# Kernel optimization log

Hardware: AMD Instinct MI355X
Metric: run time of the kernel (lower is better)

Reference implementation:

```python
import jax, jax.numpy as jnp
import numpy as np

N_NODES = 50000
N_EDGES = 600000
HIDDEN = 128
HEADS = 8
OUT_CH = HIDDEN // HEADS
NUM_LAYERS = 3
NEG_SLOPE = 0.2   # PyG GATConv default leaky_relu slope
BN_EPS = 1e-5

# Note: dropout is a no-op in eval mode; BatchNorm uses batch statistics
# (training-mode math, the only well-defined choice without running stats).

def setup_inputs() -> dict:
    key = jax.random.key(0)
    ks = jax.random.split(key, 9)
    x = jax.random.normal(ks[0], (N_NODES, HIDDEN), dtype=jnp.float32)
    edge_index = jax.random.randint(ks[1], (2, N_EDGES), 0, N_NODES, dtype=jnp.int64)
    s = 1.0 / np.sqrt(HIDDEN)
    W = jax.random.normal(ks[2], (NUM_LAYERS, HIDDEN, HEADS * OUT_CH), dtype=jnp.float32) * s
    att_src = jax.random.normal(ks[3], (NUM_LAYERS, HEADS, OUT_CH), dtype=jnp.float32) * s
    att_dst = jax.random.normal(ks[4], (NUM_LAYERS, HEADS, OUT_CH), dtype=jnp.float32) * s
    bias = jnp.zeros((NUM_LAYERS, HIDDEN), dtype=jnp.float32)
    gamma = jnp.ones((NUM_LAYERS, HIDDEN), dtype=jnp.float32)
    beta = jnp.zeros((NUM_LAYERS, HIDDEN), dtype=jnp.float32)
    return {"x": x, "edge_index": edge_index, "W": W, "att_src": att_src,
            "att_dst": att_dst, "bias": bias, "gamma": gamma, "beta": beta}


def _gat_layer(x, src, dst, W, a_src, a_dst, b):
    n = x.shape[0]
    h = (x @ W).reshape(n, HEADS, OUT_CH)              # [N,H,C]
    alpha_s = jnp.einsum('nhc,hc->nh', h, a_src)        # [N,H]
    alpha_d = jnp.einsum('nhc,hc->nh', h, a_dst)
    e = jax.nn.leaky_relu(alpha_s[src] + alpha_d[dst], NEG_SLOPE)  # [E,H]
    # segment softmax over incoming edges of each destination node
    m = jax.ops.segment_max(e, dst, num_segments=n)     # [N,H]
    e = jnp.exp(e - m[dst])
    z = jax.ops.segment_sum(e, dst, num_segments=n)
    alpha = e / (z[dst] + 1e-16)                        # [E,H]
    msg = h[src] * alpha[:, :, None]                    # [E,H,C]
    out = jax.ops.segment_sum(msg, dst, num_segments=n) # [N,H,C]
    return out.reshape(n, HEADS * OUT_CH) + b


def _batchnorm(x, gamma, beta):
    mu = x.mean(axis=0)
    var = x.var(axis=0)
    return (x - mu) * jax.lax.rsqrt(var + BN_EPS) * gamma + beta


def reference(x, edge_index, W, att_src, att_dst, bias, gamma, beta):
    src, dst = edge_index[0], edge_index[1]
    for l in range(NUM_LAYERS):
        x = _gat_layer(x, src, dst, W[l], att_src[l], att_dst[l], bias[l])
        x = _batchnorm(x, gamma[l], beta[l])
        x = jax.nn.elu(x)
    return x
```

## Files before the change

kernel.cpp:

```cpp
#include <hip/hip_runtime.h>
#include <hip/hip_bf16.h>

#define N_NODES 50000
#define N_EDGES 600000
#define HID 128
#define HEADS 8
#define OUTC 16
#define NEG_SLOPE 0.2f
#define BN_EPS 1e-5f

typedef __attribute__((ext_vector_type(8))) short short8;
typedef __attribute__((ext_vector_type(4))) float floatx4;

__device__ __forceinline__ float bf_lo(unsigned int v) { return __uint_as_float(v << 16); }
__device__ __forceinline__ float bf_hi(unsigned int v) { return __uint_as_float(v & 0xffff0000u); }

__device__ __forceinline__ short f2bfs(float v) {
    __hip_bfloat16 b = __float2bfloat16(v);
    return *reinterpret_cast<short*>(&b);
}

__global__ void k_hist_wtwa(const int* __restrict__ dst, int* __restrict__ deg, int e,
                            int nb_e, const float* __restrict__ W,
                            const float* __restrict__ asrc, const float* __restrict__ adst,
                            __hip_bfloat16* __restrict__ Wt, __hip_bfloat16* __restrict__ WAT) {
    if (blockIdx.x < (unsigned)nb_e) {
        int i = blockIdx.x * 256 + threadIdx.x;
        if (i < e) atomicAdd(&deg[dst[i]], 1);
    } else {
        int i = (blockIdx.x - nb_e) * 256 + threadIdx.x;
        if (i < 3 * 16384) {
            int l = i >> 14, r = i & 16383, n = r >> 7, k = r & 127;
            Wt[i] = __float2bfloat16(W[l * 16384 + k * 128 + n]);
        } else if (i < 3 * 16384 + 3 * 2048) {
            int q = i - 3 * 16384;
            int l = q >> 11, r = q & 2047, j = r >> 7, k = r & 127;
            const float* att = (j < 8) ? (asrc + l * 128 + j * 16) : (adst + l * 128 + (j - 8) * 16);
            const float* Wrow = W + l * 16384 + k * 128 + (j & 7) * 16;
            float sum = 0.f;
#pragma unroll
            for (int c = 0; c < 16; c++) sum += Wrow[c] * att[c];
            WAT[q] = __float2bfloat16(sum);
        }
    }
}

__global__ void k_scan1(const int* __restrict__ deg, int* __restrict__ incl,
                        int* __restrict__ partials, int n) {
    __shared__ int sh[512];
    int i = blockIdx.x * 512 + threadIdx.x;
    int v = (i < n) ? deg[i] : 0;
    sh[threadIdx.x] = v;
    __syncthreads();
    for (int off = 1; off < 512; off <<= 1) {
        int t = (threadIdx.x >= off) ? sh[threadIdx.x - off] : 0;
        __syncthreads();
        sh[threadIdx.x] += t;
        __syncthreads();
    }
    if (i < n) incl[i] = sh[threadIdx.x];
    if (threadIdx.x == 511) partials[blockIdx.x] = sh[511];
}

__global__ void k_scan2(int* __restrict__ partials, int nb) {
    __shared__ int sh[128];
    int v = (threadIdx.x < nb) ? partials[threadIdx.x] : 0;
    sh[threadIdx.x] = v;
    __syncthreads();
    for (int off = 1; off < 128; off <<= 1) {
        int t = (threadIdx.x >= off) ? sh[threadIdx.x - off] : 0;
        __syncthreads();
        sh[threadIdx.x] += t;
        __syncthreads();
    }
    if (threadIdx.x < nb) partials[threadIdx.x] = sh[threadIdx.x] - v;
}

__global__ void k_scan3(const int* __restrict__ deg, const int* __restrict__ incl,
                        const int* __restrict__ partials, int* __restrict__ row_ptr,
                        int* __restrict__ cursor, int n, int e_total) {
    int i = blockIdx.x * 512 + threadIdx.x;
    if (i < n) {
        int rp = incl[i] - deg[i] + partials[blockIdx.x];
        row_ptr[i] = rp;
        cursor[i] = rp;
    }
    if (i == 0) row_ptr[n] = e_total;
}

__global__ void k_scatter(const int* __restrict__ src, const int* __restrict__ dst,
                          int* __restrict__ cursor, int* __restrict__ col_src, int e) {
    int i = blockIdx.x * 256 + threadIdx.x;
    if (i < e) {
        int d = dst[i];
        int p = atomicAdd(&cursor[d], 1);
        col_src[p] = src[i];
    }
}

__global__ __launch_bounds__(256) void k_gemm(const float* __restrict__ Xf,
                                              const float* __restrict__ stats,
                                              const float* __restrict__ gamma,
                                              const float* __restrict__ beta,
                                              const __hip_bfloat16* __restrict__ Wt,
                                              const __hip_bfloat16* __restrict__ WAT,
                                              __hip_bfloat16* __restrict__ Hb,
                                              float* __restrict__ AS, float* __restrict__ AD,
                                              int n_nodes, int apply_bn) {
    __shared__ float s_scale[128], s_shift[128];
    if (apply_bn && threadIdx.x < 128) {
        int c = threadIdx.x;
        float invN = 1.0f / (float)N_NODES;
        float mu = stats[c] * invN;
        float var = stats[128 + c] * invN - mu * mu;
        float sc = rsqrtf(var + BN_EPS) * gamma[c];
        s_scale[c] = sc;
        s_shift[c] = beta[c] - mu * sc;
    }
    __syncthreads();

    int wave = threadIdx.x >> 6, lane = threadIdx.x & 63;
    int row0 = blockIdx.x * 64 + wave * 16;
    int m_lane = lane & 15, kq = lane >> 4;
    floatx4 acc[8] = {};
    floatx4 acc_a = {};
    const short* Ws = (const short*)Wt;
    const short* Was = (const short*)WAT;
    int r = row0 + m_lane;
    int rr = (r < n_nodes) ? r : 0;
    for (int c = 0; c < 4; c++) {
        const float4* xp = (const float4*)(Xf + (size_t)rr * 128 + c * 32 + kq * 8);
        float4 v0 = xp[0], v1 = xp[1];
        float vals[8] = {v0.x, v0.y, v0.z, v0.w, v1.x, v1.y, v1.z, v1.w};
        short8 a;
        if (apply_bn) {
            int ch0 = c * 32 + kq * 8;
#pragma unroll
            for (int j = 0; j < 8; j++) {
                float val = fmaf(vals[j], s_scale[ch0 + j], s_shift[ch0 + j]);
                val = (val > 0.f) ? val : (__expf(val) - 1.0f);
                a[j] = f2bfs(val);
            }
        } else {
#pragma unroll
            for (int j = 0; j < 8; j++)
                a[j] = f2bfs(vals[j]);
        }
        for (int t = 0; t < 8; t++) {
            short8 b = *(const short8*)(Ws + (t * 16 + m_lane) * 128 + c * 32 + kq * 8);
            acc[t] = __builtin_amdgcn_mfma_f32_16x16x32_bf16(a, b, acc[t], 0, 0, 0);
        }
        short8 bwa = *(const short8*)(Was + m_lane * 128 + c * 32 + kq * 8);
        acc_a = __builtin_amdgcn_mfma_f32_16x16x32_bf16(a, bwa, acc_a, 0, 0, 0);
    }
#pragma unroll
    for (int reg = 0; reg < 4; reg++) {
        int row = row0 + kq * 4 + reg;
        if (row >= n_nodes) continue;
#pragma unroll
        for (int t = 0; t < 8; t++)
            Hb[(size_t)row * 128 + t * 16 + m_lane] = __float2bfloat16(acc[t][reg]);
        float av = acc_a[reg];
        if (m_lane < 8) AS[row * 8 + m_lane] = av;
        else            AD[row * 8 + (m_lane - 8)] = av;
    }
}

__global__ __launch_bounds__(256) void k_agg(const int* __restrict__ RP,
                                             const int* __restrict__ COL,
                                             const float* __restrict__ AS,
                                             const float* __restrict__ AD,
                                             const __hip_bfloat16* __restrict__ Hb,
                                             float* __restrict__ out, int n_nodes) {
    int wave = threadIdx.x >> 6, lane = threadIdx.x & 63;
    int n = blockIdx.x * 4 + wave;
    if (n >= n_nodes) return;
    int e_l = lane >> 3, h = lane & 7;
    int p0 = RP[n], p1 = RP[n + 1];
    float ad = AD[n * 8 + h];
    float z = 0.f;
    float acc[16];
#pragma unroll
    for (int c = 0; c < 16; c++) acc[c] = 0.f;
    const unsigned short* Hu = (const unsigned short*)Hb;
    for (int p = p0 + e_l; p < p1; p += 8) {
        int s = COL[p];
        float e = AS[s * 8 + h] + ad;
        e = (e > 0.f) ? e : NEG_SLOPE * e;
        float w = __expf(e);
        z += w;
        const uint4* hp = (const uint4*)(Hu + (size_t)s * 128 + h * 16);
        uint4 h0 = hp[0];
        uint4 h1 = hp[1];
        unsigned int ww[8] = {h0.x, h0.y, h0.z, h0.w, h1.x, h1.y, h1.z, h1.w};
#pragma unroll
        for (int j = 0; j < 8; j++) {
            acc[2 * j]     += w * bf_lo(ww[j]);
            acc[2 * j + 1] += w * bf_hi(ww[j]);
        }
    }
#pragma unroll
    for (int off = 8; off < 64; off <<= 1) {
        z += __shfl_xor(z, off, 64);
#pragma unroll
        for (int c = 0; c < 16; c++) acc[c] += __shfl_xor(acc[c], off, 64);
    }
    if (e_l == 0) {
        float inv = 1.0f / (z + 1e-16f);
        float4* op = (float4*)(out + (size_t)n * 128 + h * 16);
#pragma unroll
        for (int q = 0; q < 4; q++) {
            op[q] = make_float4(acc[4 * q] * inv, acc[4 * q + 1] * inv,
                                acc[4 * q + 2] * inv, acc[4 * q + 3] * inv);
        }
    }
}

__global__ __launch_bounds__(256) void k_bnstats(const float* __restrict__ x,
                                                 float* __restrict__ partials,
                                                 float* __restrict__ stats,
                                                 int* __restrict__ counter, int n_nodes) {
    int tid = threadIdx.x;
    int c4 = tid & 31, sub = tid >> 5;
    int g = blockIdx.x * 8 + sub;
    float sx = 0.f, sy = 0.f, sz = 0.f, sw = 0.f;
    float qx = 0.f, qy = 0.f, qz = 0.f, qw = 0.f;
    for (int n = g; n < n_nodes; n += 2048) {
        float4 v = *(const float4*)(x + (size_t)n * 128 + c4 * 4);
        sx += v.x; sy += v.y; sz += v.z; sw += v.w;
        qx += v.x * v.x; qy += v.y * v.y; qz += v.z * v.z; qw += v.w * v.w;
    }
    __shared__ float ssum[8][128];
    __shared__ float ssq[8][128];
    int c = c4 * 4;
    ssum[sub][c] = sx; ssum[sub][c + 1] = sy; ssum[sub][c + 2] = sz; ssum[sub][c + 3] = sw;
    ssq[sub][c] = qx;  ssq[sub][c + 1] = qy;  ssq[sub][c + 2] = qz;  ssq[sub][c + 3] = qw;
    __syncthreads();
    float total = 0.f;
    if (tid < 128) {
#pragma unroll
        for (int k = 0; k < 8; k++) total += ssum[k][tid];
    } else {
        int cc = tid - 128;
#pragma unroll
        for (int k = 0; k < 8; k++) total += ssq[k][cc];
    }
    partials[blockIdx.x * 256 + tid] = total;
    __threadfence();
    __shared__ int s_last;
    if (tid == 0) s_last = (atomicAdd(counter, 1) == 255) ? 1 : 0;
    __syncthreads();
    if (s_last) {
        float s = 0.f;
#pragma unroll 8
        for (int b = 0; b < 256; b++) s += partials[b * 256 + tid];
        stats[tid] = s;
    }
}

__global__ void k_bnapply(const float* __restrict__ x, const float* __restrict__ stats,
                          const float* __restrict__ gamma, const float* __restrict__ beta,
                          float* __restrict__ outf, int n_nodes) {
    int i = blockIdx.x * 256 + threadIdx.x;
    if (i >= n_nodes * 32) return;
    float4 v = *(const float4*)(x + (size_t)i * 4);
    int c0 = (i * 4) & 127;
    float r[4] = {v.x, v.y, v.z, v.w};
    float invN = 1.0f / (float)N_NODES;
#pragma unroll
    for (int j = 0; j < 4; j++) {
        int c = c0 + j;
        float mu = stats[c] * invN;
        float var = stats[128 + c] * invN - mu * mu;
        float sc = rsqrtf(var + BN_EPS) * gamma[c];
        float val = (r[j] - mu) * sc + beta[c];
        val = (val > 0.f) ? val : (__expf(val) - 1.0f);
        r[j] = val;
    }
    *(float4*)(outf + (size_t)i * 4) = make_float4(r[0], r[1], r[2], r[3]);
}

extern "C" void kernel_launch(void* const* d_in, const int* in_sizes, int n_in,
                              void* d_out, int out_size, void* d_ws, size_t ws_size,
                              hipStream_t stream) {
    const float* x_in   = (const float*)d_in[0];
    const int*   eidx   = (const int*)d_in[1];
    const float* W      = (const float*)d_in[2];
    const float* attsrc = (const float*)d_in[3];
    const float* attdst = (const float*)d_in[4];
    const float* gamma  = (const float*)d_in[6];
    const float* beta   = (const float*)d_in[7];
    float* out = (float*)d_out;

    const int N = N_NODES, E = N_EDGES;
    const int* src = eidx;
    const int* dst = eidx + E;

    char* base = (char*)d_ws;
    size_t off = 0;
    auto carve = [&](size_t bytes) -> char* {
        char* p = base + off;
        off += (bytes + 255) & ~(size_t)255;
        return p;
    };
    __hip_bfloat16* Hb  = (__hip_bfloat16*)carve((size_t)N * HID * 2);
    float*          XN  = (float*)carve((size_t)N * HID * 4);
    float*          AS  = (float*)carve((size_t)N * HEADS * 4);
    float*          AD  = (float*)carve((size_t)N * HEADS * 4);
    __hip_bfloat16* WT  = (__hip_bfloat16*)carve((size_t)3 * HID * HID * 2);
    __hip_bfloat16* WAT = (__hip_bfloat16*)carve((size_t)3 * 16 * HID * 2);
    float*          STA = (float*)carve(3 * 256 * 4);
    float*          PAR = (float*)carve(256 * 256 * 4);
    int*            CNT = (int*)carve(256);
    int*            DEG = (int*)carve((size_t)N * 4);
    int*            INC = (int*)carve((size_t)N * 4);
    int*            RP  = (int*)carve((size_t)(N + 1) * 4);
    int*            CUR = (int*)carve((size_t)N * 4);
    int*            PRT = (int*)carve(1024 * 4);
    int*            COL = (int*)carve((size_t)E * 4);

    const int NB_E  = (E + 255) / 256;
    const int NB_SC = (N + 511) / 512;
    const int NB_W  = (3 * 16384 + 3 * 2048 + 255) / 256;

    (void)hipMemsetAsync(CNT, 0, 256 + (size_t)N * 4, stream);

    k_hist_wtwa<<<NB_E + NB_W, 256, 0, stream>>>(dst, DEG, E, NB_E, W, attsrc, attdst, WT, WAT);
    k_scan1<<<NB_SC, 512, 0, stream>>>(DEG, INC, PRT, N);
    k_scan2<<<1, 128, 0, stream>>>(PRT, NB_SC);
    k_scan3<<<NB_SC, 512, 0, stream>>>(DEG, INC, PRT, RP, CUR, N, E);
    k_scatter<<<NB_E, 256, 0, stream>>>(src, dst, CUR, COL, E);

    for (int l = 0; l < 3; l++) {
        const float* Xf = (l == 0) ? x_in : XN;
        const float* st = (l == 0) ? nullptr : (STA + (l - 1) * 256);
        const float* gm = gamma + (l - 1) * 128;
        const float* bt = beta + (l - 1) * 128;
        k_gemm<<<(N + 63) / 64, 256, 0, stream>>>(Xf, st, gm, bt,
                                                  WT + l * 16384, WAT + l * 2048,
                                                  Hb, AS, AD, N, (l == 0) ? 0 : 1);
        k_agg<<<(N + 3) / 4, 256, 0, stream>>>(RP, COL, AS, AD, Hb, XN, N);
        k_bnstats<<<256, 256, 0, stream>>>(XN, PAR, STA + l * 256, CNT + l, N);
    }
    k_bnapply<<<(N * 32 + 255) / 256, 256, 0, stream>>>(XN, STA + 2 * 256,
                                                        gamma + 2 * 128, beta + 2 * 128, out, N);
}
```

Before: 433.8 us.

## Fuse whole GAT pipeline into one cooperative persistent kernel with grid syncs

```diff
diff --git a/kernel.cpp b/kernel.cpp
--- a/kernel.cpp
+++ b/kernel.cpp
@@ -1,5 +1,8 @@
 #include <hip/hip_runtime.h>
 #include <hip/hip_bf16.h>
+#include <hip/hip_cooperative_groups.h>
+
+namespace cg = cooperative_groups;
 
 #define N_NODES 50000
 #define N_EDGES 600000
@@ -18,6 +21,284 @@
 __device__ __forceinline__ short f2bfs(float v) {
     __hip_bfloat16 b = __float2bfloat16(v);
     return *reinterpret_cast<short*>(&b);
+}
+
+struct MegaParams {
+    const float* x_in;
+    const int* src;
+    const int* dst;
+    const float* W;
+    const float* asrc;
+    const float* adst;
+    const float* gamma;
+    const float* beta;
+    float* out;
+    __hip_bfloat16* Hb;
+    float* XN;
+    float* AS;
+    float* AD;
+    __hip_bfloat16* WT;
+    __hip_bfloat16* WAT;
+    float* STA;
+    float* PAR;
+    int* CNT;
+    int* DEG;
+    int* INC;
+    int* RP;
+    int* CUR;
+    int* PRT;
+    int* COL;
+};
+
+__global__ __launch_bounds__(256, 3) void k_mega(MegaParams P) {
+    cg::grid_group grid = cg::this_grid();
+    const int nb = gridDim.x;
+    const int bid = blockIdx.x;
+    const int tid = threadIdx.x;
+    const int gthreads = nb * 256;
+    const int gtid = bid * 256 + tid;
+
+    __shared__ int s_scan[256];
+    __shared__ float s_scale[128], s_shift[128];
+    __shared__ float ssum[8][128], ssq[8][128];
+    __shared__ int s_last;
+
+    for (int i = gtid; i < N_NODES; i += gthreads) P.DEG[i] = 0;
+    if (gtid < 3) P.CNT[gtid] = 0;
+    for (int i = gtid; i < 3 * 16384 + 3 * 2048; i += gthreads) {
+        if (i < 3 * 16384) {
+            int l = i >> 14, r = i & 16383, n = r >> 7, k = r & 127;
+            P.WT[i] = __float2bfloat16(P.W[l * 16384 + k * 128 + n]);
+        } else {
+            int q = i - 3 * 16384;
+            int l = q >> 11, r = q & 2047, j = r >> 7, k = r & 127;
+            const float* att = (j < 8) ? (P.asrc + l * 128 + j * 16)
+                                       : (P.adst + l * 128 + (j - 8) * 16);
+            const float* Wrow = P.W + l * 16384 + k * 128 + (j & 7) * 16;
+            float sum = 0.f;
+#pragma unroll
+            for (int c = 0; c < 16; c++) sum += Wrow[c] * att[c];
+            P.WAT[q] = __float2bfloat16(sum);
+        }
+    }
+    grid.sync();
+
+    for (int i = gtid; i < N_EDGES; i += gthreads) atomicAdd(&P.DEG[P.dst[i]], 1);
+    grid.sync();
+
+    const int NVB = (N_NODES + 255) / 256;
+    for (int vb = bid; vb < NVB; vb += nb) {
+        int i = vb * 256 + tid;
+        int v = (i < N_NODES) ? P.DEG[i] : 0;
+        s_scan[tid] = v;
+        __syncthreads();
+        for (int off = 1; off < 256; off <<= 1) {
+            int t = (tid >= off) ? s_scan[tid - off] : 0;
+            __syncthreads();
+            s_scan[tid] += t;
+            __syncthreads();
+        }
+        if (i < N_NODES) P.INC[i] = s_scan[tid];
+        if (tid == 255) P.PRT[vb] = s_scan[255];
+        __syncthreads();
+    }
+    grid.sync();
+
+    if (bid == 0) {
+        int v = (tid < NVB) ? P.PRT[tid] : 0;
+        s_scan[tid] = v;
+        __syncthreads();
+        for (int off = 1; off < 256; off <<= 1) {
+            int t = (tid >= off) ? s_scan[tid - off] : 0;
+            __syncthreads();
+            s_scan[tid] += t;
+            __syncthreads();
+        }
+        if (tid < NVB) P.PRT[tid] = s_scan[tid] - v;
+    }
+    grid.sync();
+
+    for (int i = gtid; i < N_NODES; i += gthreads) {
+        int rp = P.INC[i] - P.DEG[i] + P.PRT[i >> 8];
+        P.RP[i] = rp;
+        P.CUR[i] = rp;
+    }
+    if (gtid == 0) P.RP[N_NODES] = N_EDGES;
+    grid.sync();
+
+    for (int i = gtid; i < N_EDGES; i += gthreads) {
+        int d = P.dst[i];
+        int p = atomicAdd(&P.CUR[d], 1);
+        P.COL[p] = P.src[i];
+    }
+    grid.sync();
+
+    const int wave = tid >> 6, lane = tid & 63;
+    const int m_lane = lane & 15, kq = lane >> 4;
+    for (int l = 0; l < 3; l++) {
+        if (l > 0 && tid < 128) {
+            const float* stats = P.STA + (l - 1) * 256;
+            float invN = 1.0f / (float)N_NODES;
+            float mu = stats[tid] * invN;
+            float var = stats[128 + tid] * invN - mu * mu;
+            float sc = rsqrtf(var + BN_EPS) * P.gamma[(l - 1) * 128 + tid];
+            s_scale[tid] = sc;
+            s_shift[tid] = P.beta[(l - 1) * 128 + tid] - mu * sc;
+        }
+        __syncthreads();
+
+        const float* Xf = (l == 0) ? P.x_in : P.XN;
+        const short* Ws = (const short*)(P.WT + l * 16384);
+        const short* Was = (const short*)(P.WAT + l * 2048);
+        const int NT = (N_NODES + 63) / 64;
+        for (int vt = bid; vt < NT; vt += nb) {
+            int row0 = vt * 64 + wave * 16;
+            floatx4 acc[8] = {};
+            floatx4 acc_a = {};
+            int r = row0 + m_lane;
+            int rr = (r < N_NODES) ? r : 0;
+            for (int c = 0; c < 4; c++) {
+                const float4* xp = (const float4*)(Xf + (size_t)rr * 128 + c * 32 + kq * 8);
+                float4 v0 = xp[0], v1 = xp[1];
+                float vals[8] = {v0.x, v0.y, v0.z, v0.w, v1.x, v1.y, v1.z, v1.w};
+                short8 a;
+                if (l > 0) {
+                    int ch0 = c * 32 + kq * 8;
+#pragma unroll
+                    for (int j = 0; j < 8; j++) {
+                        float val = fmaf(vals[j], s_scale[ch0 + j], s_shift[ch0 + j]);
+                        val = (val > 0.f) ? val : (__expf(val) - 1.0f);
+                        a[j] = f2bfs(val);
+                    }
+                } else {
+#pragma unroll
+                    for (int j = 0; j < 8; j++) a[j] = f2bfs(vals[j]);
+                }
+                for (int t = 0; t < 8; t++) {
+                    short8 b = *(const short8*)(Ws + (t * 16 + m_lane) * 128 + c * 32 + kq * 8);
+                    acc[t] = __builtin_amdgcn_mfma_f32_16x16x32_bf16(a, b, acc[t], 0, 0, 0);
+                }
+                short8 bwa = *(const short8*)(Was + m_lane * 128 + c * 32 + kq * 8);
+                acc_a = __builtin_amdgcn_mfma_f32_16x16x32_bf16(a, bwa, acc_a, 0, 0, 0);
+            }
+#pragma unroll
+            for (int reg = 0; reg < 4; reg++) {
+                int row = row0 + kq * 4 + reg;
+                if (row >= N_NODES) continue;
+#pragma unroll
+                for (int t = 0; t < 8; t++)
+                    P.Hb[(size_t)row * 128 + t * 16 + m_lane] = __float2bfloat16(acc[t][reg]);
+                float av = acc_a[reg];
+                if (m_lane < 8) P.AS[row * 8 + m_lane] = av;
+                else            P.AD[row * 8 + (m_lane - 8)] = av;
+            }
+        }
+        grid.sync();
+
+        const int NG = (N_NODES + 3) / 4;
+        const unsigned short* Hu = (const unsigned short*)P.Hb;
+        for (int vg = bid; vg < NG; vg += nb) {
+            int n = vg * 4 + wave;
+            if (n >= N_NODES) continue;
+            int e_l = lane >> 3, h = lane & 7;
+            int p0 = P.RP[n], p1 = P.RP[n + 1];
+            float ad = P.AD[n * 8 + h];
+            float z = 0.f;
+            float acc[16];
+#pragma unroll
+            for (int c = 0; c < 16; c++) acc[c] = 0.f;
+            for (int p = p0 + e_l; p < p1; p += 8) {
+                int s = P.COL[p];
+                float e = P.AS[s * 8 + h] + ad;
+                e = (e > 0.f) ? e : NEG_SLOPE * e;
+                float w = __expf(e);
+                z += w;
+                const uint4* hp = (const uint4*)(Hu + (size_t)s * 128 + h * 16);
+                uint4 h0 = hp[0];
+                uint4 h1 = hp[1];
+                unsigned int ww[8] = {h0.x, h0.y, h0.z, h0.w, h1.x, h1.y, h1.z, h1.w};
+#pragma unroll
+                for (int j = 0; j < 8; j++) {
+                    acc[2 * j]     += w * bf_lo(ww[j]);
+                    acc[2 * j + 1] += w * bf_hi(ww[j]);
+                }
+            }
+#pragma unroll
+            for (int off = 8; off < 64; off <<= 1) {
+                z += __shfl_xor(z, off, 64);
+#pragma unroll
+                for (int c = 0; c < 16; c++) acc[c] += __shfl_xor(acc[c], off, 64);
+            }
+            if (e_l == 0) {
+                float inv = 1.0f / (z + 1e-16f);
+                float4* op = (float4*)(P.XN + (size_t)n * 128 + h * 16);
+#pragma unroll
+                for (int q = 0; q < 4; q++)
+                    op[q] = make_float4(acc[4 * q] * inv, acc[4 * q + 1] * inv,
+                                        acc[4 * q + 2] * inv, acc[4 * q + 3] * inv);
+            }
+        }
+        grid.sync();
+
+        if (bid < 256) {
+            int c4 = tid & 31, sub = tid >> 5;
+            int g = bid * 8 + sub;
+            float sx = 0.f, sy = 0.f, sz = 0.f, sw = 0.f;
+            float qx = 0.f, qy = 0.f, qz = 0.f, qw = 0.f;
+            for (int n = g; n < N_NODES; n += 2048) {
+                float4 v = *(const float4*)(P.XN + (size_t)n * 128 + c4 * 4);
+                sx += v.x; sy += v.y; sz += v.z; sw += v.w;
+                qx += v.x * v.x; qy += v.y * v.y; qz += v.z * v.z; qw += v.w * v.w;
+            }
+            int c = c4 * 4;
+            ssum[sub][c] = sx; ssum[sub][c + 1] = sy; ssum[sub][c + 2] = sz; ssum[sub][c + 3] = sw;
+            ssq[sub][c] = qx;  ssq[sub][c + 1] = qy;  ssq[sub][c + 2] = qz;  ssq[sub][c + 3] = qw;
+            __syncthreads();
+            float total = 0.f;
+            if (tid < 128) {
+#pragma unroll
+                for (int k = 0; k < 8; k++) total += ssum[k][tid];
+            } else {
+                int cc = tid - 128;
+#pragma unroll
+                for (int k = 0; k < 8; k++) total += ssq[k][cc];
+            }
+            P.PAR[bid * 256 + tid] = total;
+            __threadfence();
+            if (tid == 0) s_last = (atomicAdd(P.CNT + l, 1) == 255) ? 1 : 0;
+            __syncthreads();
+            if (s_last) {
+                float s = 0.f;
+#pragma unroll 8
+                for (int b = 0; b < 256; b++) s += P.PAR[b * 256 + tid];
+                P.STA[l * 256 + tid] = s;
+            }
+        }
+        grid.sync();
+    }
+
+    {
+        const float* stats = P.STA + 2 * 256;
+        const float* gm = P.gamma + 2 * 128;
+        const float* bt = P.beta + 2 * 128;
+        float invN = 1.0f / (float)N_NODES;
+        for (int i = gtid; i < N_NODES * 32; i += gthreads) {
+            float4 v = *(const float4*)(P.XN + (size_t)i * 4);
+            int c0 = (i * 4) & 127;
+            float r[4] = {v.x, v.y, v.z, v.w};
+#pragma unroll
+            for (int j = 0; j < 4; j++) {
+                int c = c0 + j;
+                float mu = stats[c] * invN;
+                float var = stats[128 + c] * invN - mu * mu;
+                float sc = rsqrtf(var + BN_EPS) * gm[c];
+                float val = (r[j] - mu) * sc + bt[c];
+                val = (val > 0.f) ? val : (__expf(val) - 1.0f);
+                r[j] = val;
+            }
+            *(float4*)(P.out + (size_t)i * 4) = make_float4(r[0], r[1], r[2], r[3]);
+        }
+    }
 }
 
 __global__ void k_hist_wtwa(const int* __restrict__ dst, int* __restrict__ deg, int e,
@@ -118,7 +399,6 @@
         s_shift[c] = beta[c] - mu * sc;
     }
     __syncthreads();
-
     int wave = threadIdx.x >> 6, lane = threadIdx.x & 63;
     int row0 = blockIdx.x * 64 + wave * 16;
     int m_lane = lane & 15, kq = lane >> 4;
@@ -143,8 +423,7 @@
             }
         } else {
 #pragma unroll
-            for (int j = 0; j < 8; j++)
-                a[j] = f2bfs(vals[j]);
+            for (int j = 0; j < 8; j++) a[j] = f2bfs(vals[j]);
         }
         for (int t = 0; t < 8; t++) {
             short8 b = *(const short8*)(Ws + (t * 16 + m_lane) * 128 + c * 32 + kq * 8);
@@ -209,10 +488,9 @@
         float inv = 1.0f / (z + 1e-16f);
         float4* op = (float4*)(out + (size_t)n * 128 + h * 16);
 #pragma unroll
-        for (int q = 0; q < 4; q++) {
+        for (int q = 0; q < 4; q++)
             op[q] = make_float4(acc[4 * q] * inv, acc[4 * q + 1] * inv,
                                 acc[4 * q + 2] * inv, acc[4 * q + 3] * inv);
-        }
     }
 }
 
@@ -319,12 +597,23 @@
     int*            PRT = (int*)carve(1024 * 4);
     int*            COL = (int*)carve((size_t)E * 4);
 
+    MegaParams P = { x_in, src, dst, W, attsrc, attdst, gamma, beta, out,
+                     Hb, XN, AS, AD, WT, WAT, STA, PAR, CNT, DEG, INC, RP, CUR, PRT, COL };
+    int perCU = 0;
+    hipError_t qerr = hipOccupancyMaxActiveBlocksPerMultiprocessor(
+        &perCU, reinterpret_cast<const void*>(k_mega), 256, 0);
+    int grid = (qerr == hipSuccess && perCU > 0) ? perCU * 256 : 768;
+    if (grid > 2048) grid = 2048;
+    void* args[] = { (void*)&P };
+    hipError_t lerr = hipLaunchCooperativeKernel(reinterpret_cast<const void*>(k_mega),
+                                                 dim3(grid), dim3(256), args, 0, stream);
+    if (lerr == hipSuccess) return;
+
     const int NB_E  = (E + 255) / 256;
     const int NB_SC = (N + 511) / 512;
     const int NB_W  = (3 * 16384 + 3 * 2048 + 255) / 256;
 
     (void)hipMemsetAsync(CNT, 0, 256 + (size_t)N * 4, stream);
-
     k_hist_wtwa<<<NB_E + NB_W, 256, 0, stream>>>(dst, DEG, E, NB_E, W, attsrc, attdst, WT, WAT);
     k_scan1<<<NB_SC, 512, 0, stream>>>(DEG, INC, PRT, N);
     k_scan2<<<1, 128, 0, stream>>>(PRT, NB_SC);
```

Measured after the change: 1.391 ms. 221% more time.

## Switch node features to head-major layout and aggregate per head

Applied to the files above, without the earlier changes.

```diff
diff --git a/kernel.cpp b/kernel.cpp
--- a/kernel.cpp
+++ b/kernel.cpp
@@ -14,6 +14,7 @@
 
 __device__ __forceinline__ float bf_lo(unsigned int v) { return __uint_as_float(v << 16); }
 __device__ __forceinline__ float bf_hi(unsigned int v) { return __uint_as_float(v & 0xffff0000u); }
+__device__ __forceinline__ float bf1(unsigned short v) { return __uint_as_float((unsigned int)v << 16); }
 
 __device__ __forceinline__ short f2bfs(float v) {
     __hip_bfloat16 b = __float2bfloat16(v);
@@ -104,7 +105,7 @@
                                               const float* __restrict__ beta,
                                               const __hip_bfloat16* __restrict__ Wt,
                                               const __hip_bfloat16* __restrict__ WAT,
-                                              __hip_bfloat16* __restrict__ Hb,
+                                              __hip_bfloat16* __restrict__ Hh,
                                               float* __restrict__ AS, float* __restrict__ AD,
                                               int n_nodes, int apply_bn) {
     __shared__ float s_scale[128], s_shift[128];
@@ -143,8 +144,7 @@
             }
         } else {
 #pragma unroll
-            for (int j = 0; j < 8; j++)
-                a[j] = f2bfs(vals[j]);
+            for (int j = 0; j < 8; j++) a[j] = f2bfs(vals[j]);
         }
         for (int t = 0; t < 8; t++) {
             short8 b = *(const short8*)(Ws + (t * 16 + m_lane) * 128 + c * 32 + kq * 8);
@@ -159,10 +159,10 @@
         if (row >= n_nodes) continue;
 #pragma unroll
         for (int t = 0; t < 8; t++)
-            Hb[(size_t)row * 128 + t * 16 + m_lane] = __float2bfloat16(acc[t][reg]);
+            Hh[((size_t)t * n_nodes + row) * 16 + m_lane] = __float2bfloat16(acc[t][reg]);
         float av = acc_a[reg];
-        if (m_lane < 8) AS[row * 8 + m_lane] = av;
-        else            AD[row * 8 + (m_lane - 8)] = av;
+        if (m_lane < 8) AS[(size_t)m_lane * n_nodes + row] = av;
+        else            AD[(size_t)(m_lane - 8) * n_nodes + row] = av;
     }
 }
 
@@ -170,49 +170,37 @@
                                              const int* __restrict__ COL,
                                              const float* __restrict__ AS,
                                              const float* __restrict__ AD,
-                                             const __hip_bfloat16* __restrict__ Hb,
+                                             const __hip_bfloat16* __restrict__ Hh,
                                              float* __restrict__ out, int n_nodes) {
     int wave = threadIdx.x >> 6, lane = threadIdx.x & 63;
-    int n = blockIdx.x * 4 + wave;
-    if (n >= n_nodes) return;
-    int e_l = lane >> 3, h = lane & 7;
-    int p0 = RP[n], p1 = RP[n + 1];
-    float ad = AD[n * 8 + h];
-    float z = 0.f;
-    float acc[16];
-#pragma unroll
-    for (int c = 0; c < 16; c++) acc[c] = 0.f;
-    const unsigned short* Hu = (const unsigned short*)Hb;
-    for (int p = p0 + e_l; p < p1; p += 8) {
-        int s = COL[p];
-        float e = AS[s * 8 + h] + ad;
-        e = (e > 0.f) ? e : NEG_SLOPE * e;
-        float w = __expf(e);
-        z += w;
-        const uint4* hp = (const uint4*)(Hu + (size_t)s * 128 + h * 16);
-        uint4 h0 = hp[0];
-        uint4 h1 = hp[1];
-        unsigned int ww[8] = {h0.x, h0.y, h0.z, h0.w, h1.x, h1.y, h1.z, h1.w};
-#pragma unroll
-        for (int j = 0; j < 8; j++) {
-            acc[2 * j]     += w * bf_lo(ww[j]);
-            acc[2 * j + 1] += w * bf_hi(ww[j]);
-        }
-    }
-#pragma unroll
-    for (int off = 8; off < 64; off <<= 1) {
-        z += __shfl_xor(z, off, 64);
-#pragma unroll
-        for (int c = 0; c < 16; c++) acc[c] += __shfl_xor(acc[c], off, 64);
-    }
-    if (e_l == 0) {
-        float inv = 1.0f / (z + 1e-16f);
-        float4* op = (float4*)(out + (size_t)n * 128 + h * 16);
-#pragma unroll
-        for (int q = 0; q < 4; q++) {
-            op[q] = make_float4(acc[4 * q] * inv, acc[4 * q + 1] * inv,
-                                acc[4 * q + 2] * inv, acc[4 * q + 3] * inv);
-        }
+    int h = blockIdx.x / 6250;
+    int g = blockIdx.x % 6250;
+    int e_l = lane >> 4, c = lane & 15;
+    const unsigned short* Hu = (const unsigned short*)(Hh + (size_t)h * n_nodes * 16);
+    const float* ASh = AS + (size_t)h * n_nodes;
+    const float* ADh = AD + (size_t)h * n_nodes;
+#pragma unroll
+    for (int nn = 0; nn < 2; nn++) {
+        int n = g * 8 + wave * 2 + nn;
+        if (n >= n_nodes) continue;
+        int p0 = RP[n], p1 = RP[n + 1];
+        float ad = ADh[n];
+        float z = 0.f, acc = 0.f;
+        for (int p = p0 + e_l; p < p1; p += 4) {
+            int s = COL[p];
+            float e = ASh[s] + ad;
+            e = (e > 0.f) ? e : NEG_SLOPE * e;
+            float w = __expf(e);
+            z += w;
+            acc += w * bf1(Hu[(size_t)s * 16 + c]);
+        }
+#pragma unroll
+        for (int off = 16; off < 64; off <<= 1) {
+            z += __shfl_xor(z, off, 64);
+            acc += __shfl_xor(acc, off, 64);
+        }
+        if (e_l == 0)
+            out[(size_t)n * 128 + h * 16 + c] = acc / (z + 1e-16f);
     }
 }
 
@@ -303,7 +291,7 @@
         off += (bytes + 255) & ~(size_t)255;
         return p;
     };
-    __hip_bfloat16* Hb  = (__hip_bfloat16*)carve((size_t)N * HID * 2);
+    __hip_bfloat16* Hh  = (__hip_bfloat16*)carve((size_t)N * HID * 2);
     float*          XN  = (float*)carve((size_t)N * HID * 4);
     float*          AS  = (float*)carve((size_t)N * HEADS * 4);
     float*          AD  = (float*)carve((size_t)N * HEADS * 4);
@@ -338,8 +326,8 @@
         const float* bt = beta + (l - 1) * 128;
         k_gemm<<<(N + 63) / 64, 256, 0, stream>>>(Xf, st, gm, bt,
                                                   WT + l * 16384, WAT + l * 2048,
-                                                  Hb, AS, AD, N, (l == 0) ? 0 : 1);
-        k_agg<<<(N + 3) / 4, 256, 0, stream>>>(RP, COL, AS, AD, Hb, XN, N);
+                                                  Hh, AS, AD, N, (l == 0) ? 0 : 1);
+        k_agg<<<8 * 6250, 256, 0, stream>>>(RP, COL, AS, AD, Hh, XN, N);
         k_bnstats<<<256, 256, 0, stream>>>(XN, PAR, STA + l * 256, CNT + l, N);
     }
     k_bnapply<<<(N * 32 + 255) / 256, 256, 0, stream>>>(XN, STA + 2 * 256,
```

Measured after the change: 737.1 us. 1.7x slower.
